# Performance work log

Hardware: AMD Instinct MI355X
Metric: run time of the kernel (lower is better)

Reference implementation:

```python
import jax, jax.numpy as jnp
import numpy as np

B, C, PC, P = 64, 32, 128, 2048
N = B * C * PC          # 262144 graph nodes
E = 2097152             # ~8 edges per node


def _gcn(x, src, dst, n, W, b):
    # PyG GCNConv: add self loops, sym-normalized mean aggregation of x@W
    xw = x @ W
    sl = jnp.arange(n, dtype=src.dtype)
    s = jnp.concatenate([src, sl]); d = jnp.concatenate([dst, sl])
    deg = jax.ops.segment_sum(jnp.ones(d.shape, xw.dtype), d, num_segments=n)
    dinv = jax.lax.rsqrt(deg)  # deg >= 1 thanks to self loops
    norm = dinv[s] * dinv[d]
    return jax.ops.segment_sum(xw[s] * norm[:, None], d, num_segments=n) + b


def _gat(x, src, dst, n, W, a_src, a_dst, b):
    # PyG GATConv (heads=1): self loops, edge softmax over incoming edges
    xw = x @ W
    sl = jnp.arange(n, dtype=src.dtype)
    s = jnp.concatenate([src, sl]); d = jnp.concatenate([dst, sl])
    e = jax.nn.leaky_relu((xw @ a_src)[s] + (xw @ a_dst)[d], 0.2)
    m = jax.ops.segment_max(jax.lax.stop_gradient(e), d, num_segments=n)
    ex = jnp.exp(e - m[d])
    denom = jax.ops.segment_sum(ex, d, num_segments=n)
    alpha = ex / denom[d]
    return jax.ops.segment_sum(xw[s] * alpha[:, None], d, num_segments=n) + b


def _cross_edges(num_cross, batch_size):
    # faithful to get_c_adjacency: every ordered pair (i!=j) appears twice per graph
    ii, jj = np.meshgrid(np.arange(num_cross), np.arange(num_cross), indexing='ij')
    m = ii != jj
    s, d = ii[m], jj[m]
    s2 = np.concatenate([s, d]); d2 = np.concatenate([d, s])
    off = (np.arange(batch_size) * num_cross)[:, None]
    src = (s2[None] + off).reshape(-1)
    dst = (d2[None] + off).reshape(-1)
    return jnp.asarray(src, jnp.int32), jnp.asarray(dst, jnp.int32)


def _conv1d(x, W, b):
    y = jax.lax.conv_general_dilated(x, W, (2,), ((1, 1),), dimension_numbers=('NCH', 'OIH', 'NCH'))
    return y + b[None, :, None]


def _bn_eval(x, gamma, beta):
    # BatchNorm1d in eval mode with default running stats (mean 0, var 1)
    scale = gamma / np.float32(np.sqrt(1.0 + 1e-5))
    return x * scale[None, :, None] + beta[None, :, None]


def setup_inputs() -> dict:
    key = jax.random.key(0)
    ks = jax.random.split(key, 32)
    rn = lambda k, sh, s=0.1: (jax.random.normal(k, sh, jnp.float32) * s)
    return {
        'x': jax.random.normal(ks[0], (N, 19), jnp.float32),
        'edge_index': jax.random.randint(ks[1], (2, E), 0, N, jnp.int32),
        'points': jax.random.normal(ks[2], (B, 3, P), jnp.float32),
        'W1': rn(ks[3], (19, 32)), 'b1': rn(ks[4], (32,)),
        'W2': rn(ks[5], (32, 64)), 'b2': rn(ks[6], (64,)),
        'W3': rn(ks[7], (64, 64)), 'b3': rn(ks[8], (64,)),
        'Wg1': rn(ks[9], (64, 64)), 'asrc1': rn(ks[10], (64,)), 'adst1': rn(ks[11], (64,)), 'bg1': rn(ks[12], (64,)),
        'Wg2': rn(ks[13], (64, 64)), 'asrc2': rn(ks[14], (64,)), 'adst2': rn(ks[15], (64,)), 'bg2': rn(ks[16], (64,)),
        'c1W': rn(ks[17], (32, 3, 3)), 'c1b': rn(ks[18], (32,)),
        'g1': 1.0 + rn(ks[19], (32,)), 'be1': rn(ks[20], (32,)),
        'c2W': rn(ks[21], (64, 32, 3)), 'c2b': rn(ks[22], (64,)),
        'g2': 1.0 + rn(ks[23], (64,)), 'be2': rn(ks[24], (64,)),
        'c3W': rn(ks[25], (64, 64, 3)), 'c3b': rn(ks[26], (64,)),
        'Wl2': rn(ks[27], (64, 64)), 'bl2': rn(ks[28], (64,)),
        'Wl3': rn(ks[29], (64, 1)), 'bl3': rn(ks[30], (1,)),
        'batch_size': B, 'num_cross': C, 'num_pieces': PC,
    }


def reference(x, edge_index, points, W1, b1, W2, b2, W3, b3,
              Wg1, asrc1, adst1, bg1, Wg2, asrc2, adst2, bg2,
              c1W, c1b, g1, be1, c2W, c2b, g2, be2, c3W, c3b,
              Wl2, bl2, Wl3, bl3, batch_size, num_cross, num_pieces):
    src, dst = edge_index[0], edge_index[1]
    n = x.shape[0]
    h = jax.nn.relu(_gcn(x, src, dst, n, W1, b1))  # dropout is a no-op in eval
    h = jax.nn.leaky_relu(_gcn(h, src, dst, n, W2, b2), 0.01)
    h = jax.nn.leaky_relu(_gcn(h, src, dst, n, W3, b3), 0.01)
    h = _gat(h, src, dst, n, Wg1, asrc1, adst1, bg1)
    h = h.reshape(batch_size, num_cross, num_pieces, -1).mean(-2)  # [B, C, 64]
    s2, d2 = _cross_edges(num_cross, batch_size)
    h = _gat(h.reshape(batch_size * num_cross, 64), s2, d2, batch_size * num_cross, Wg2, asrc2, adst2, bg2)
    h = h.reshape(batch_size, num_cross, 64).mean(1)  # [B, 64]
    p = _bn_eval(jax.nn.leaky_relu(_conv1d(points, c1W, c1b), 0.01), g1, be1)
    p = _bn_eval(jax.nn.leaky_relu(_conv1d(p, c2W, c2b), 0.01), g2, be2)
    p = jax.nn.leaky_relu(_conv1d(p, c3W, c3b), 0.01).mean(-1)  # AdaptiveAvgPool1d(1).squeeze -> [B, 64]
    h = h + p
    h = jax.nn.leaky_relu(h @ Wl2 + bl2, 0.01)
    return jax.nn.sigmoid(h @ Wl3 + bl3)  # [B, 1]
```

## Files before the change

### kernel.cpp

```cpp
#include <hip/hip_runtime.h>
#include <cstdint>
#include <cstddef>

#define NN 262144
#define EE 2097152
#define BB 64
#define CCROSS 32
#define PCC 128
#define PP 2048
#define NBUCK 256
#define BCAP 12288

typedef _Float16 f16;
typedef __attribute__((ext_vector_type(2))) _Float16 f16x2;
typedef __attribute__((ext_vector_type(4))) _Float16 f16x4;
typedef __attribute__((ext_vector_type(8))) _Float16 f16x8;
typedef __attribute__((ext_vector_type(4))) float f32x4;

static __device__ __forceinline__ float lrelu(float x, float s) { return x > 0.f ? x : s * x; }

#if __has_builtin(__builtin_amdgcn_fdot2)
static __device__ __forceinline__ float dot2f(unsigned x, unsigned w, float c) {
    return __builtin_amdgcn_fdot2(__builtin_bit_cast(f16x2, x), __builtin_bit_cast(f16x2, w), c, false);
}
#else
static __device__ __forceinline__ float dot2f(unsigned x, unsigned w, float c) {
    f16x2 a = __builtin_bit_cast(f16x2, x);
    f16x2 b = __builtin_bit_cast(f16x2, w);
    return fmaf((float)a[0], (float)b[0], fmaf((float)a[1], (float)b[1], c));
}
#endif

__global__ __launch_bounds__(256) void bucket_a_k(const int* __restrict__ src, const int* __restrict__ dst,
                                                  unsigned* __restrict__ buckets, int* __restrict__ gcnt) {
    __shared__ int hist[NBUCK];
    __shared__ int base[NBUCK];
    __shared__ unsigned short rankbuf[8192];
    const int tid = threadIdx.x;
    const int e0 = blockIdx.x * 8192;
    hist[tid] = 0;
    __syncthreads();
    for (int i = tid; i < 8192; i += 256) {
        int d = dst[e0 + i];
        rankbuf[i] = (unsigned short)atomicAdd(&hist[d >> 10], 1);
    }
    __syncthreads();
    base[tid] = tid * BCAP + atomicAdd(&gcnt[tid], hist[tid]);
    __syncthreads();
    for (int i = tid; i < 8192; i += 256) {
        int s = src[e0 + i];
        int d = dst[e0 + i];
        int b = d >> 10;
        buckets[base[b] + rankbuf[i]] = ((unsigned)s << 10) | (unsigned)(d & 1023);
    }
}

__global__ void bucket_scan_k(const int* __restrict__ gcnt, int* __restrict__ bbase, int* __restrict__ rp) {
    __shared__ int tmp[256];
    int tid = threadIdx.x;
    int v = gcnt[tid];
    tmp[tid] = v;
    __syncthreads();
    for (int off = 1; off < 256; off <<= 1) {
        int t = (tid >= off) ? tmp[tid - off] : 0;
        __syncthreads();
        tmp[tid] += t;
        __syncthreads();
    }
    bbase[tid] = tmp[tid] - v;
    if (tid == 0) rp[NN] = EE;
}

__global__ __launch_bounds__(256) void bucket_b_k(const unsigned* __restrict__ buckets, const int* __restrict__ gcnt,
                                                  const int* __restrict__ bbase, int* __restrict__ rp,
                                                  float* __restrict__ dinv, int* __restrict__ col) {
    __shared__ int cnt[1024];
    __shared__ int scan[1024];
    __shared__ int wsum[256];
    const int b = blockIdx.x;
    const int tid = threadIdx.x;
    int n = gcnt[b];
    if (n > BCAP) n = BCAP;
    const unsigned* eb = buckets + (size_t)b * BCAP;
    const int gb = bbase[b];
    for (int i = tid; i < 1024; i += 256) cnt[i] = 0;
    __syncthreads();
    for (int i = tid; i < n; i += 256) atomicAdd(&cnt[eb[i] & 1023], 1);
    __syncthreads();
    int b4 = tid * 4;
    int c0 = cnt[b4], c1 = cnt[b4 + 1], c2 = cnt[b4 + 2], c3 = cnt[b4 + 3];
    int tsum = c0 + c1 + c2 + c3;
    wsum[tid] = tsum;
    __syncthreads();
    for (int off = 1; off < 256; off <<= 1) {
        int t = (tid >= off) ? wsum[tid - off] : 0;
        __syncthreads();
        wsum[tid] += t;
        __syncthreads();
    }
    int excl = wsum[tid] - tsum;
    scan[b4] = excl;
    scan[b4 + 1] = excl + c0;
    scan[b4 + 2] = excl + c0 + c1;
    scan[b4 + 3] = excl + c0 + c1 + c2;
    int vbase = b * 1024 + b4;
    rp[vbase + 0] = gb + scan[b4 + 0];
    rp[vbase + 1] = gb + scan[b4 + 1];
    rp[vbase + 2] = gb + scan[b4 + 2];
    rp[vbase + 3] = gb + scan[b4 + 3];
    dinv[vbase + 0] = rsqrtf((float)(c0 + 1));
    dinv[vbase + 1] = rsqrtf((float)(c1 + 1));
    dinv[vbase + 2] = rsqrtf((float)(c2 + 1));
    dinv[vbase + 3] = rsqrtf((float)(c3 + 1));
    __syncthreads();
    for (int i = tid; i < 1024; i += 256) cnt[i] = 0;
    __syncthreads();
    for (int i = tid; i < n; i += 256) {
        unsigned p = eb[i];
        int dl = p & 1023;
        int r = atomicAdd(&cnt[dl], 1);
        col[gb + scan[dl] + r] = (int)(p >> 10);
    }
}

__global__ void zprep_k(const float* __restrict__ x, const float* __restrict__ dinv, f16* __restrict__ z) {
    int v = blockIdx.x * 256 + threadIdx.x;
    if (v >= NN) return;
    float dv = dinv[v];
    const float* xr = x + (size_t)v * 19;
    float vv[20];
#pragma unroll
    for (int k = 0; k < 19; k++) vv[k] = dv * xr[k];
    vv[19] = 0.f;
    f16x4* zr = (f16x4*)(z + (size_t)v * 32);
#pragma unroll
    for (int c = 0; c < 5; c++) {
        f16x4 t = {(f16)vv[4 * c], (f16)vv[4 * c + 1], (f16)vv[4 * c + 2], (f16)vv[4 * c + 3]};
        zr[c] = t;
    }
    f16x4 zz = {(f16)0.f, (f16)0.f, (f16)0.f, (f16)0.f};
#pragma unroll
    for (int c = 5; c < 8; c++) zr[c] = zz;
}

#define ZSTR1 36
template <int KINR, int KOUT, int ACT>
__global__ __launch_bounds__(256) void fused_agg_gemm_k(const f16* __restrict__ z, const int* __restrict__ rp,
                                                        const int* __restrict__ col, const float* __restrict__ Wg,
                                                        const float* __restrict__ dinv, const float* __restrict__ bias,
                                                        f16* __restrict__ zout) {
    constexpr int NO = KOUT / 4;
    __shared__ float Wl[32 * KOUT];
    __shared__ float zrow[64 * ZSTR1];
    const int tid = threadIdx.x;
    for (int i = tid; i < 32 * KOUT; i += 256) Wl[i] = (i < KINR * KOUT) ? Wg[i] : 0.f;

    const int r = tid >> 2;
    const int idx = tid & 3;
    const int v = blockIdx.x * 64 + r;
    const f16x8* z8 = (const f16x8*)z;
    f16x8 a = z8[(size_t)v * 4 + idx];
    float acc8[8];
#pragma unroll
    for (int j = 0; j < 8; j++) acc8[j] = (float)a[j];
    int st = rp[v], e = rp[v + 1];
    int i = st;
    for (; i + 4 <= e; i += 4) {
        int u0 = col[i], u1 = col[i + 1], u2 = col[i + 2], u3 = col[i + 3];
        f16x8 a0 = z8[(size_t)u0 * 4 + idx];
        f16x8 a1 = z8[(size_t)u1 * 4 + idx];
        f16x8 a2 = z8[(size_t)u2 * 4 + idx];
        f16x8 a3 = z8[(size_t)u3 * 4 + idx];
#pragma unroll
        for (int j = 0; j < 8; j++)
            acc8[j] += ((float)a0[j] + (float)a1[j]) + ((float)a2[j] + (float)a3[j]);
    }
    for (; i < e; i++) {
        f16x8 aa = z8[(size_t)col[i] * 4 + idx];
#pragma unroll
        for (int j = 0; j < 8; j++) acc8[j] += (float)aa[j];
    }
    float4 s0, s1;
    s0.x = acc8[0]; s0.y = acc8[1]; s0.z = acc8[2]; s0.w = acc8[3];
    s1.x = acc8[4]; s1.y = acc8[5]; s1.z = acc8[6]; s1.w = acc8[7];
    *(float4*)&zrow[r * ZSTR1 + idx * 8] = s0;
    *(float4*)&zrow[r * ZSTR1 + idx * 8 + 4] = s1;
    __syncthreads();

    float acc[NO];
#pragma unroll
    for (int j = 0; j < NO; j++) acc[j] = 0.f;
#pragma unroll 4
    for (int k = 0; k < 32; k++) {
        float zv = zrow[r * ZSTR1 + k];
        const float* wr = Wl + k * KOUT + NO * idx;
#pragma unroll
        for (int j = 0; j < NO; j++) acc[j] = fmaf(zv, wr[j], acc[j]);
    }
    float dv = dinv[v];
    f16 hv[NO];
#pragma unroll
    for (int j = 0; j < NO; j++) {
        float o = dv * acc[j] + bias[NO * idx + j];
        o = (ACT == 0) ? fmaxf(o, 0.f) : lrelu(o, 0.01f);
        hv[j] = (f16)(o * dv);
    }
    if constexpr (NO == 8) {
        f16x8 h = {hv[0], hv[1], hv[2], hv[3], hv[4], hv[5], hv[6], hv[7]};
        *(f16x8*)(zout + (size_t)v * KOUT + NO * idx) = h;
    } else {
        f16x8 h0 = {hv[0], hv[1], hv[2], hv[3], hv[4], hv[5], hv[6], hv[7]};
        f16x8 h1 = {hv[8], hv[9], hv[10], hv[11], hv[12], hv[13], hv[14], hv[15]};
        f16x8* yo = (f16x8*)(zout + (size_t)v * KOUT + NO * idx);
        yo[0] = h0; yo[1] = h1;
    }
}

__global__ void pack_w_k(const float* __restrict__ W, f16* __restrict__ out) {
    int o = blockIdx.x * 256 + threadIdx.x;
    if (o >= 4096) return;
    int frag = o >> 9;
    int kt = frag >> 2;
    int c = frag & 3;
    int idx = o & 511;
    int l = idx >> 3;
    int j = idx & 7;
    int k = kt * 32 + ((l >> 4) << 3) + j;
    int n = 16 * c + (l & 15);
    out[o] = (f16)W[k * 64 + n];
}

__global__ void pack_c2_k(const float* __restrict__ W, f16* __restrict__ out) {
    int o = blockIdx.x * 256 + threadIdx.x;
    if (o >= 64 * 96) return;
    int ch = o / 96, r = o - ch * 96;
    int k = r >> 5, ci = r & 31;
    out[o] = (f16)W[ch * 96 + ci * 3 + k];
}

__global__ void pack_c3_k(const float* __restrict__ W, f16* __restrict__ out) {
    int o = blockIdx.x * 256 + threadIdx.x;
    if (o >= 64 * 192) return;
    int ch = o / 192, r = o - ch * 192;
    int k = r >> 6, ci = r & 63;
    out[o] = (f16)W[ch * 192 + ci * 3 + k];
}

#define HSTR 72
__global__ __launch_bounds__(256) void gemm3_gat_k(const f16* __restrict__ y, const int* __restrict__ rp,
                                                   const int* __restrict__ col, const f16* __restrict__ w3p,
                                                   const float* __restrict__ dinv, const float* __restrict__ b3,
                                                   const f16* __restrict__ wgp, const float* __restrict__ av,
                                                   const float* __restrict__ ad, f16* __restrict__ xw,
                                                   float* __restrict__ es, float* __restrict__ ed) {
    __shared__ f16 zin[64 * HSTR];
    __shared__ f16 hh[64 * HSTR];
    const int tid = threadIdx.x;
    const int v0 = blockIdx.x * 64;
    {
        const int row = tid >> 2;
        const int idx = tid & 3;
        const int v = v0 + row;
        const f16x8* y8 = (const f16x8*)y;
        f16x8 s0 = y8[(size_t)v * 8 + idx * 2];
        f16x8 s1 = y8[(size_t)v * 8 + idx * 2 + 1];
        float acc[16];
#pragma unroll
        for (int j = 0; j < 8; j++) { acc[j] = (float)s0[j]; acc[8 + j] = (float)s1[j]; }
        int s = rp[v], e = rp[v + 1];
        int i = s;
        for (; i + 2 <= e; i += 2) {
            int u0 = col[i], u1 = col[i + 1];
            f16x8 a0 = y8[(size_t)u0 * 8 + idx * 2];
            f16x8 a1 = y8[(size_t)u0 * 8 + idx * 2 + 1];
            f16x8 b0 = y8[(size_t)u1 * 8 + idx * 2];
            f16x8 b1 = y8[(size_t)u1 * 8 + idx * 2 + 1];
#pragma unroll
            for (int j = 0; j < 8; j++) {
                acc[j] += (float)a0[j] + (float)b0[j];
                acc[8 + j] += (float)a1[j] + (float)b1[j];
            }
        }
        for (; i < e; i++) {
            int u = col[i];
            f16x8 a0 = y8[(size_t)u * 8 + idx * 2];
            f16x8 a1 = y8[(size_t)u * 8 + idx * 2 + 1];
#pragma unroll
            for (int j = 0; j < 8; j++) { acc[j] += (float)a0[j]; acc[8 + j] += (float)a1[j]; }
        }
        f16x8 o0, o1;
#pragma unroll
        for (int j = 0; j < 8; j++) { o0[j] = (f16)acc[j]; o1[j] = (f16)acc[8 + j]; }
        *(f16x8*)&zin[row * HSTR + idx * 16] = o0;
        *(f16x8*)&zin[row * HSTR + idx * 16 + 8] = o1;
    }
    __syncthreads();

    const int w = tid >> 6;
    const int l = tid & 63;
    const int m = l & 15;
    const int q = l >> 4;
    const int r0 = 16 * w;

    f32x4 acc0 = {0.f, 0.f, 0.f, 0.f}, acc1 = acc0, acc2 = acc0, acc3 = acc0;
#pragma unroll
    for (int kt = 0; kt < 2; kt++) {
        f16x8 afrag = *(const f16x8*)&zin[(r0 + m) * HSTR + kt * 32 + q * 8];
        f16x8 b0 = *(const f16x8*)&w3p[((kt * 4 + 0) << 9) + l * 8];
        f16x8 b1 = *(const f16x8*)&w3p[((kt * 4 + 1) << 9) + l * 8];
        f16x8 b2 = *(const f16x8*)&w3p[((kt * 4 + 2) << 9) + l * 8];
        f16x8 b3f = *(const f16x8*)&w3p[((kt * 4 + 3) << 9) + l * 8];
        acc0 = __builtin_amdgcn_mfma_f32_16x16x32_f16(afrag, b0, acc0, 0, 0, 0);
        acc1 = __builtin_amdgcn_mfma_f32_16x16x32_f16(afrag, b1, acc1, 0, 0, 0);
        acc2 = __builtin_amdgcn_mfma_f32_16x16x32_f16(afrag, b2, acc2, 0, 0, 0);
        acc3 = __builtin_amdgcn_mfma_f32_16x16x32_f16(afrag, b3f, acc3, 0, 0, 0);
    }
    {
        float dv0 = dinv[v0 + r0 + q * 4 + 0];
        float dv1 = dinv[v0 + r0 + q * 4 + 1];
        float dv2 = dinv[v0 + r0 + q * 4 + 2];
        float dv3 = dinv[v0 + r0 + q * 4 + 3];
#pragma unroll
        for (int c = 0; c < 4; c++) {
            const f32x4* ac = (c == 0) ? &acc0 : (c == 1) ? &acc1 : (c == 2) ? &acc2 : &acc3;
            float bb = b3[16 * c + m];
            hh[(r0 + q * 4 + 0) * HSTR + 16 * c + m] = (f16)lrelu(dv0 * (*ac)[0] + bb, 0.01f);
            hh[(r0 + q * 4 + 1) * HSTR + 16 * c + m] = (f16)lrelu(dv1 * (*ac)[1] + bb, 0.01f);
            hh[(r0 + q * 4 + 2) * HSTR + 16 * c + m] = (f16)lrelu(dv2 * (*ac)[2] + bb, 0.01f);
            hh[(r0 + q * 4 + 3) * HSTR + 16 * c + m] = (f16)lrelu(dv3 * (*ac)[3] + bb, 0.01f);
        }
    }
    __syncthreads();

    acc0 = (f32x4){0.f, 0.f, 0.f, 0.f}; acc1 = acc0; acc2 = acc0; acc3 = acc0;
#pragma unroll
    for (int kt = 0; kt < 2; kt++) {
        f16x8 afrag = *(const f16x8*)&hh[(r0 + m) * HSTR + kt * 32 + q * 8];
        f16x8 b0 = *(const f16x8*)&wgp[((kt * 4 + 0) << 9) + l * 8];
        f16x8 b1 = *(const f16x8*)&wgp[((kt * 4 + 1) << 9) + l * 8];
        f16x8 b2 = *(const f16x8*)&wgp[((kt * 4 + 2) << 9) + l * 8];
        f16x8 b3f = *(const f16x8*)&wgp[((kt * 4 + 3) << 9) + l * 8];
        acc0 = __builtin_amdgcn_mfma_f32_16x16x32_f16(afrag, b0, acc0, 0, 0, 0);
        acc1 = __builtin_amdgcn_mfma_f32_16x16x32_f16(afrag, b1, acc1, 0, 0, 0);
        acc2 = __builtin_amdgcn_mfma_f32_16x16x32_f16(afrag, b2, acc2, 0, 0, 0);
        acc3 = __builtin_amdgcn_mfma_f32_16x16x32_f16(afrag, b3f, acc3, 0, 0, 0);
    }
    {
        float e1[4] = {0.f, 0.f, 0.f, 0.f}, e2[4] = {0.f, 0.f, 0.f, 0.f};
#pragma unroll
        for (int c = 0; c < 4; c++) {
            const f32x4* ac = (c == 0) ? &acc0 : (c == 1) ? &acc1 : (c == 2) ? &acc2 : &acc3;
            float a1 = av[16 * c + m];
            float d1 = ad[16 * c + m];
#pragma unroll
            for (int reg = 0; reg < 4; reg++) {
                float g = (*ac)[reg];
                e1[reg] = fmaf(g, a1, e1[reg]);
                e2[reg] = fmaf(g, d1, e2[reg]);
                xw[(size_t)(v0 + r0 + q * 4 + reg) * 64 + 16 * c + m] = (f16)g;
            }
        }
#pragma unroll
        for (int reg = 0; reg < 4; reg++) {
            e1[reg] += __shfl_xor(e1[reg], 1); e1[reg] += __shfl_xor(e1[reg], 2);
            e1[reg] += __shfl_xor(e1[reg], 4); e1[reg] += __shfl_xor(e1[reg], 8);
            e2[reg] += __shfl_xor(e2[reg], 1); e2[reg] += __shfl_xor(e2[reg], 2);
            e2[reg] += __shfl_xor(e2[reg], 4); e2[reg] += __shfl_xor(e2[reg], 8);
        }
        if (m == 0) {
#pragma unroll
            for (int reg = 0; reg < 4; reg++) {
                es[v0 + r0 + q * 4 + reg] = e1[reg];
                ed[v0 + r0 + q * 4 + reg] = e2[reg];
            }
        }
    }
}

__global__ void gat_w_k(const float* __restrict__ es, const float* __restrict__ ed,
                        const int* __restrict__ rp, const int* __restrict__ col,
                        f16* __restrict__ ewi, float* __restrict__ wsi) {
    int v = blockIdx.x * 256 + threadIdx.x;
    if (v >= NN) return;
    float edv = ed[v];
    float eself = lrelu(es[v] + edv, 0.2f);
    float m = eself;
    int s = rp[v], e = rp[v + 1];
    int i = s;
    float lg[32];
    for (; i + 4 <= e; i += 4) {
        int u0 = col[i], u1 = col[i + 1], u2 = col[i + 2], u3 = col[i + 3];
        float t0 = lrelu(es[u0] + edv, 0.2f);
        float t1 = lrelu(es[u1] + edv, 0.2f);
        float t2 = lrelu(es[u2] + edv, 0.2f);
        float t3 = lrelu(es[u3] + edv, 0.2f);
        int k = i - s;
        if (k + 3 < 32) { lg[k] = t0; lg[k + 1] = t1; lg[k + 2] = t2; lg[k + 3] = t3; }
        m = fmaxf(m, fmaxf(fmaxf(t0, t1), fmaxf(t2, t3)));
    }
    for (; i < e; i++) {
        float t = lrelu(es[col[i]] + edv, 0.2f);
        int k = i - s;
        if (k < 32) lg[k] = t;
        m = fmaxf(m, t);
    }
    float wsl = __expf(eself - m);
    float den = wsl;
    for (i = s; i < e; i++) {
        int k = i - s;
        float t = (k < 32) ? lg[k] : lrelu(es[col[i]] + edv, 0.2f);
        float w = __expf(t - m);
        if (k < 32) lg[k] = w;
        den += w;
    }
    float inv = 1.f / den;
    for (i = s; i < e; i++) {
        int k = i - s;
        float w = (k < 32) ? lg[k] : __expf(lrelu(es[col[i]] + edv, 0.2f) - m);
        ewi[i] = (f16)(w * inv);
    }
    wsi[v] = wsl * inv;
}

__global__ __launch_bounds__(256) void gat_agg_pool_k(const f16* __restrict__ y, const int* __restrict__ rp,
                                                      const int* __restrict__ col, const f16* __restrict__ ewi,
                                                      const float* __restrict__ wsi,
                                                      const float* __restrict__ bias, float* __restrict__ pooled) {
    __shared__ float sred[32 * 68];
    const int g = blockIdx.x;
    const int tid = threadIdx.x;
    const int idx = tid & 7;
    const int slot = tid >> 3;
    const f16x8* y8 = (const f16x8*)y;
    float acc[8];
#pragma unroll
    for (int j = 0; j < 8; j++) acc[j] = 0.f;

#pragma unroll
    for (int pass = 0; pass < 4; pass++) {
        const int v = g * 128 + pass * 32 + slot;
        float ws = wsi[v];
        f16x8 self = y8[(size_t)v * 8 + idx];
#pragma unroll
        for (int j = 0; j < 8; j++) acc[j] = fmaf(ws, (float)self[j], acc[j]);
    }

    const int s = rp[g * 128];
    const int e = rp[g * 128 + 128];
    int i = s + slot;
    for (; i + 96 < e; i += 128) {
        int u0 = col[i], u1 = col[i + 32], u2 = col[i + 64], u3 = col[i + 96];
        float w0 = (float)ewi[i], w1 = (float)ewi[i + 32], w2 = (float)ewi[i + 64], w3 = (float)ewi[i + 96];
        f16x8 a0 = y8[(size_t)u0 * 8 + idx];
        f16x8 a1 = y8[(size_t)u1 * 8 + idx];
        f16x8 a2 = y8[(size_t)u2 * 8 + idx];
        f16x8 a3 = y8[(size_t)u3 * 8 + idx];
#pragma unroll
        for (int j = 0; j < 8; j++)
            acc[j] = fmaf(w0, (float)a0[j], fmaf(w1, (float)a1[j], fmaf(w2, (float)a2[j], fmaf(w3, (float)a3[j], acc[j]))));
    }
    for (; i < e; i += 32) {
        int u = col[i];
        float w = (float)ewi[i];
        f16x8 a = y8[(size_t)u * 8 + idx];
#pragma unroll
        for (int j = 0; j < 8; j++) acc[j] = fmaf(w, (float)a[j], acc[j]);
    }

#pragma unroll
    for (int j = 0; j < 8; j++) sred[slot * 68 + idx * 8 + j] = acc[j];
    __syncthreads();
    if (tid < 64) {
        float s2 = 0.f;
#pragma unroll
        for (int k = 0; k < 32; k++) s2 += sred[k * 68 + tid];
        pooled[(size_t)g * 64 + tid] = s2 * (1.f / 128.f) + bias[tid];
    }
}

__global__ void pool_cross_k(const float* __restrict__ in, float* __restrict__ out) {
    int gid = blockIdx.x * 64 + threadIdx.x;
    if (gid >= BB * 64) return;
    int f = gid & 63, b = gid >> 6;
    const float* p = in + (size_t)b * CCROSS * 64 + f;
    float s = 0.f;
#pragma unroll
    for (int i = 0; i < CCROSS; i++) s += p[(size_t)i * 64];
    out[gid] = s * (1.f / 32.f);
}

template <int KIN, int KOUT>
__global__ void gat_gemm_k(const float* __restrict__ x, const float* __restrict__ W,
                           float* __restrict__ y, const float* __restrict__ av, const float* __restrict__ ad,
                           float* __restrict__ es, float* __restrict__ ed, int n) {
    int v = blockIdx.x * 256 + threadIdx.x;
    if (v >= n) return;
    const float* xr = x + (size_t)v * KIN;
    float acc[KOUT];
#pragma unroll
    for (int j = 0; j < KOUT; j++) acc[j] = 0.f;
#pragma unroll 2
    for (int k = 0; k < KIN; k++) {
        float xv = xr[k];
#pragma unroll
        for (int j = 0; j < KOUT; j++) acc[j] = fmaf(xv, W[k * KOUT + j], acc[j]);
    }
    float e1 = 0.f, e2 = 0.f;
    float4* y4 = (float4*)(y + (size_t)v * KOUT);
#pragma unroll
    for (int j4 = 0; j4 < KOUT / 4; j4++) {
        float4 t;
        t.x = acc[4 * j4 + 0]; t.y = acc[4 * j4 + 1]; t.z = acc[4 * j4 + 2]; t.w = acc[4 * j4 + 3];
        y4[j4] = t;
        e1 = fmaf(t.x, av[4 * j4 + 0], e1); e1 = fmaf(t.y, av[4 * j4 + 1], e1);
        e1 = fmaf(t.z, av[4 * j4 + 2], e1); e1 = fmaf(t.w, av[4 * j4 + 3], e1);
        e2 = fmaf(t.x, ad[4 * j4 + 0], e2); e2 = fmaf(t.y, ad[4 * j4 + 1], e2);
        e2 = fmaf(t.z, ad[4 * j4 + 2], e2); e2 = fmaf(t.w, ad[4 * j4 + 3], e2);
    }
    es[v] = e1; ed[v] = e2;
}

__global__ void cross_att_k(const float* __restrict__ xw, const float* __restrict__ es,
                            const float* __restrict__ ed, const float* __restrict__ bg,
                            float* __restrict__ out) {
    int gid = blockIdx.x * 256 + threadIdx.x;
    if (gid >= BB * CCROSS * 64) return;
    int f = gid & 63;
    int d = (gid >> 6) & 31;
    int g = gid >> 11;
    int base = g * CCROSS;
    float edd = ed[base + d];
    float m = -1e30f;
#pragma unroll
    for (int s = 0; s < CCROSS; s++) {
        float e = lrelu(es[base + s] + edd, 0.2f);
        m = fmaxf(m, e);
    }
    float den = 0.f, acc = 0.f;
#pragma unroll
    for (int s = 0; s < CCROSS; s++) {
        float e = lrelu(es[base + s] + edd, 0.2f);
        float w = __expf(e - m) * ((s == d) ? 1.f : 2.f);
        den += w;
        acc = fmaf(w, xw[(size_t)(base + s) * 64 + f], acc);
    }
    out[gid] = acc / den + bg[f];
}

__global__ __launch_bounds__(256) void conv_fused_k(
        const float* __restrict__ pts, const float* __restrict__ c1W, const float* __restrict__ c1b,
        const float* __restrict__ g1, const float* __restrict__ be1,
        const f16* __restrict__ w2p, const float* __restrict__ c2b,
        const float* __restrict__ g2, const float* __restrict__ be2,
        const f16* __restrict__ w3pc, const float* __restrict__ c3b,
        float* __restrict__ partials) {
    __shared__ __align__(16) float s0[3 * 264];
    __shared__ __align__(16) f16 s1T[132 * 32];
    __shared__ __align__(16) f16 s2T[66 * 64];
    __shared__ float sred[256];

    const int b = blockIdx.x >> 3;
    const int q = blockIdx.x & 7;
    const int tid = threadIdx.x;
    const float bnscale = 0.99999500003749968f;

    const int lo0 = 256 * q - 7;
    for (int t = tid; t < 3 * 263; t += 256) {
        int c = t / 263, j = t - c * 263;
        int p = lo0 + j;
        s0[c * 264 + j] = (p >= 0 && p < PP) ? pts[((size_t)b * 3 + c) * PP + p] : 0.f;
    }
    __syncthreads();

    {
        const int ch = tid & 31;
        const int j0 = tid >> 5;
        float wv[9];
        const float* wg = c1W + ch * 9;
#pragma unroll
        for (int t = 0; t < 9; t++) wv[t] = wg[t];
        const float bs = c1b[ch];
        const float gs = g1[ch] * bnscale;
        const float bt = be1[ch];
        const int lo1 = 128 * q - 3;
        for (int j = j0; j < 131; j += 8) {
            int p1 = lo1 + j;
            float v = 0.f;
            if (p1 >= 0 && p1 < 1024) {
                const float* x0 = s0 + 2 * j;
                float a0 = bs, a1 = 0.f, a2 = 0.f;
#pragma unroll
                for (int c = 0; c < 3; c++) {
                    float2 x01 = *(const float2*)(x0 + c * 264);
                    float x2v = x0[c * 264 + 2];
                    a0 = fmaf(x01.x, wv[c * 3 + 0], a0);
                    a1 = fmaf(x01.y, wv[c * 3 + 1], a1);
                    a2 = fmaf(x2v, wv[c * 3 + 2], a2);
                }
                float acc = a0 + a1 + a2;
                acc = lrelu(acc, 0.01f);
                v = fmaf(acc, gs, bt);
            }
            s1T[j * 32 + ch] = (f16)v;
        }
    }
    __syncthreads();

    {
        const int ch = tid & 63;
        const int jg = tid >> 6;
        unsigned wr[48];
        const uint4* wp = (const uint4*)(w2p + (size_t)ch * 96);
#pragma unroll
        for (int t = 0; t < 12; t++) {
            uint4 u = wp[t];
            wr[4 * t + 0] = u.x; wr[4 * t + 1] = u.y; wr[4 * t + 2] = u.z; wr[4 * t + 3] = u.w;
        }
        const float bs = c2b[ch];
        const float gs = g2[ch] * bnscale;
        const float bt = be2[ch];
        const int lo2v = 64 * q - 1;
        for (int j = jg; j < 65; j += 4) {
            float ak[3] = {bs, 0.f, 0.f};
#pragma unroll
            for (int k = 0; k < 3; k++) {
                const uint4* xp = (const uint4*)(s1T + (2 * j + k) * 32);
                uint4 x0 = xp[0], x1 = xp[1], x2 = xp[2], x3 = xp[3];
                float a = ak[k];
                a = dot2f(x0.x, wr[k * 16 + 0], a);
                a = dot2f(x0.y, wr[k * 16 + 1], a);
                a = dot2f(x0.z, wr[k * 16 + 2], a);
                a = dot2f(x0.w, wr[k * 16 + 3], a);
                a = dot2f(x1.x, wr[k * 16 + 4], a);
                a = dot2f(x1.y, wr[k * 16 + 5], a);
                a = dot2f(x1.z, wr[k * 16 + 6], a);
                a = dot2f(x1.w, wr[k * 16 + 7], a);
                a = dot2f(x2.x, wr[k * 16 + 8], a);
                a = dot2f(x2.y, wr[k * 16 + 9], a);
                a = dot2f(x2.z, wr[k * 16 + 10], a);
                a = dot2f(x2.w, wr[k * 16 + 11], a);
                a = dot2f(x3.x, wr[k * 16 + 12], a);
                a = dot2f(x3.y, wr[k * 16 + 13], a);
                a = dot2f(x3.z, wr[k * 16 + 14], a);
                a = dot2f(x3.w, wr[k * 16 + 15], a);
                ak[k] = a;
            }
            float acc = ak[0] + ak[1] + ak[2];
            int p2 = lo2v + j;
            float v = 0.f;
            if (p2 >= 0 && p2 < 512) v = fmaf(lrelu(acc, 0.01f), gs, bt);
            s2T[j * 64 + ch] = (f16)v;
        }
    }
    __syncthreads();

    {
        const int ch = tid & 63;
        const int jg = tid >> 6;
        unsigned wr[96];
        const uint4* wp = (const uint4*)(w3pc + (size_t)ch * 192);
#pragma unroll
        for (int t = 0; t < 24; t++) {
            uint4 u = wp[t];
            wr[4 * t + 0] = u.x; wr[4 * t + 1] = u.y; wr[4 * t + 2] = u.z; wr[4 * t + 3] = u.w;
        }
        const float bs = c3b[ch];
        float psum = 0.f;
        for (int j = jg; j < 32; j += 4) {
            float ak[3] = {bs, 0.f, 0.f};
#pragma unroll
            for (int k = 0; k < 3; k++) {
                const uint4* xp = (const uint4*)(s2T + (2 * j + k) * 64);
                float a = ak[k];
#pragma unroll
                for (int t = 0; t < 8; t++) {
                    uint4 xv = xp[t];
                    a = dot2f(xv.x, wr[k * 32 + 4 * t + 0], a);
                    a = dot2f(xv.y, wr[k * 32 + 4 * t + 1], a);
                    a = dot2f(xv.z, wr[k * 32 + 4 * t + 2], a);
                    a = dot2f(xv.w, wr[k * 32 + 4 * t + 3], a);
                }
                ak[k] = a;
            }
            psum += lrelu(ak[0] + ak[1] + ak[2], 0.01f);
        }
        sred[tid] = psum;
    }
    __syncthreads();
    if (tid < 64) {
        float s = sred[tid] + sred[tid + 64] + sred[tid + 128] + sred[tid + 192];
        partials[((size_t)b * 8 + q) * 64 + tid] = s;
    }
}

__global__ void head_k(const float* __restrict__ hG, const float* __restrict__ partials,
                       const float* __restrict__ Wl2, const float* __restrict__ bl2,
                       const float* __restrict__ Wl3, const float* __restrict__ bl3,
                       float* __restrict__ out) {
    int b = blockIdx.x;
    int f = threadIdx.x;
    __shared__ float sh[64];
    float p = 0.f;
#pragma unroll
    for (int q = 0; q < 8; q++) p += partials[((size_t)b * 8 + q) * 64 + f];
    float h = hG[b * 64 + f] + p * (1.f / 256.f);
    sh[f] = h;
    __syncthreads();
    float acc = bl2[f];
#pragma unroll
    for (int k = 0; k < 64; k++) acc = fmaf(sh[k], Wl2[k * 64 + f], acc);
    acc = lrelu(acc, 0.01f);
    float pr = acc * Wl3[f];
#pragma unroll
    for (int off = 32; off > 0; off >>= 1) pr += __shfl_down(pr, off, 64);
    if (f == 0) out[b] = 1.f / (1.f + __expf(-(pr + bl3[0])));
}

extern "C" void kernel_launch(void* const* d_in, const int* in_sizes, int n_in,
                              void* d_out, int out_size, void* d_ws, size_t ws_size,
                              hipStream_t stream) {
    const float* x = (const float*)d_in[0];
    const int* ei = (const int*)d_in[1];
    const float* points = (const float*)d_in[2];
    const float* W1 = (const float*)d_in[3];
    const float* b1 = (const float*)d_in[4];
    const float* W2 = (const float*)d_in[5];
    const float* b2 = (const float*)d_in[6];
    const float* W3 = (const float*)d_in[7];
    const float* b3 = (const float*)d_in[8];
    const float* Wg1 = (const float*)d_in[9];
    const float* asrc1 = (const float*)d_in[10];
    const float* adst1 = (const float*)d_in[11];
    const float* bg1 = (const float*)d_in[12];
    const float* Wg2 = (const float*)d_in[13];
    const float* asrc2 = (const float*)d_in[14];
    const float* adst2 = (const float*)d_in[15];
    const float* bg2 = (const float*)d_in[16];
    const float* c1W = (const float*)d_in[17];
    const float* c1b = (const float*)d_in[18];
    const float* g1 = (const float*)d_in[19];
    const float* be1 = (const float*)d_in[20];
    const float* c2W = (const float*)d_in[21];
    const float* c2b = (const float*)d_in[22];
    const float* g2 = (const float*)d_in[23];
    const float* be2 = (const float*)d_in[24];
    const float* c3W = (const float*)d_in[25];
    const float* c3b = (const float*)d_in[26];
    const float* Wl2 = (const float*)d_in[27];
    const float* bl2 = (const float*)d_in[28];
    const float* Wl3 = (const float*)d_in[29];
    const float* bl3 = (const float*)d_in[30];

    const int* src = ei;
    const int* dst = ei + EE;

    char* w = (char*)d_ws;
    size_t off = 0;
    auto A = [&](size_t bytes) -> void* {
        void* p = w + off;
        off = (off + bytes + 255) & ~(size_t)255;
        return p;
    };
    int* colb = (int*)A((size_t)EE * 4);
    int* rp = (int*)A((size_t)(NN + 1) * 4);
    int* gcnt = (int*)A(NBUCK * 4);
    int* bbase = (int*)A(NBUCK * 4);
    float* dinv = (float*)A((size_t)NN * 4);
    float* bufA = (float*)A((size_t)NN * 64 * 4);
    f16* bufH1 = (f16*)A((size_t)NN * 64 * 2);
    f16* bufH2 = (f16*)A((size_t)NN * 64 * 2);
    f16* ewi = (f16*)A((size_t)EE * 2);
    float* wsi = (float*)A((size_t)NN * 4);
    float* es = (float*)A((size_t)NN * 4);
    float* edv = (float*)A((size_t)NN * 4);
    f16* w3p = (f16*)A(4096 * 2);
    f16* wgp = (f16*)A(4096 * 2);
    f16* wc2p = (f16*)A(64 * 96 * 2);
    f16* wc3p = (f16*)A(64 * 192 * 2);
    float* pooled = (float*)A((size_t)BB * CCROSS * 64 * 4);
    float* xw2 = (float*)A((size_t)BB * CCROSS * 64 * 4);
    float* es2 = (float*)A((size_t)BB * CCROSS * 4);
    float* ed2 = (float*)A((size_t)BB * CCROSS * 4);
    float* crosso = (float*)A((size_t)BB * CCROSS * 64 * 4);
    float* hG = (float*)A((size_t)BB * 64 * 4);
    float* partials = (float*)A((size_t)BB * 8 * 64 * 4);

    unsigned* buckets = (unsigned*)bufA;

    hipMemsetAsync(gcnt, 0, NBUCK * 4, stream);
    bucket_a_k<<<EE / 8192, 256, 0, stream>>>(src, dst, buckets, gcnt);
    bucket_scan_k<<<1, 256, 0, stream>>>(gcnt, bbase, rp);
    bucket_b_k<<<NBUCK, 256, 0, stream>>>(buckets, gcnt, bbase, rp, dinv, colb);

    pack_c2_k<<<24, 256, 0, stream>>>(c2W, wc2p);
    pack_c3_k<<<48, 256, 0, stream>>>(c3W, wc3p);
    conv_fused_k<<<BB * 8, 256, 0, stream>>>(points, c1W, c1b, g1, be1, wc2p, c2b, g2, be2, wc3p, c3b, partials);
    pack_w_k<<<16, 256, 0, stream>>>(W3, w3p);
    pack_w_k<<<16, 256, 0, stream>>>(Wg1, wgp);

    zprep_k<<<NN / 256, 256, 0, stream>>>(x, dinv, bufH1);
    fused_agg_gemm_k<19, 32, 0><<<NN / 64, 256, 0, stream>>>(bufH1, rp, colb, W1, dinv, b1, bufH2);
    fused_agg_gemm_k<32, 64, 1><<<NN / 64, 256, 0, stream>>>(bufH2, rp, colb, W2, dinv, b2, bufH1);
    gemm3_gat_k<<<NN / 64, 256, 0, stream>>>(bufH1, rp, colb, w3p, dinv, b3, wgp, asrc1, adst1,
                                             bufH2, es, edv);

    gat_w_k<<<NN / 256, 256, 0, stream>>>(es, edv, rp, colb, ewi, wsi);
    gat_agg_pool_k<<<BB * CCROSS, 256, 0, stream>>>(bufH2, rp, colb, ewi, wsi, bg1, pooled);

    gat_gemm_k<64, 64><<<(BB * CCROSS) / 256, 256, 0, stream>>>(pooled, Wg2, xw2, asrc2, adst2, es2, ed2, BB * CCROSS);
    cross_att_k<<<(BB * CCROSS * 64) / 256, 256, 0, stream>>>(xw2, es2, ed2, bg2, crosso);
    pool_cross_k<<<BB, 64, 0, stream>>>(crosso, hG);

    head_k<<<BB, 64, 0, stream>>>(hG, partials, Wl2, bl2, Wl3, bl3, (float*)d_out);
}
```

Before: 473.8 us.

## Balance edge aggregation across threads with edge-chunked split and LDS float atomics

The neighbor gather in the fused GCN3+GAT kernel now splits the block's CSR edge range evenly across 32 slots of 8 threads each, instead of giving each node to 4 threads. Each slot finds its starting row by binary search over a shared copy of the row pointers, sums per-row partials, and adds them into an fp32 LDS buffer with atomics. The goal is to remove load imbalance from uneven node degrees and to issue more independent gathers per thread. In exchange it adds LDS atomics, an extra fp32 staging pass, another barrier and more shared memory, though hh now reuses the fp32 buffer.

After: 572.2 us. 1.21x slower.

```diff
diff --git a/kernel.cpp b/kernel.cpp
--- a/kernel.cpp
+++ b/kernel.cpp
@@ -247,52 +247,78 @@
 }
 
 #define HSTR 72
+#define Z32S 68
 __global__ __launch_bounds__(256) void gemm3_gat_k(const f16* __restrict__ y, const int* __restrict__ rp,
                                                    const int* __restrict__ col, const f16* __restrict__ w3p,
                                                    const float* __restrict__ dinv, const float* __restrict__ b3,
                                                    const f16* __restrict__ wgp, const float* __restrict__ av,
                                                    const float* __restrict__ ad, f16* __restrict__ xw,
                                                    float* __restrict__ es, float* __restrict__ ed) {
+    __shared__ float zin32[64 * Z32S];
     __shared__ f16 zin[64 * HSTR];
-    __shared__ f16 hh[64 * HSTR];
+    __shared__ int rpl[65];
+    f16* hh = (f16*)zin32;
+
     const int tid = threadIdx.x;
     const int v0 = blockIdx.x * 64;
+    const f16x8* y8 = (const f16x8*)y;
+
+    if (tid < 65) rpl[tid] = rp[v0 + tid];
     {
-        const int row = tid >> 2;
-        const int idx = tid & 3;
-        const int v = v0 + row;
-        const f16x8* y8 = (const f16x8*)y;
-        f16x8 s0 = y8[(size_t)v * 8 + idx * 2];
-        f16x8 s1 = y8[(size_t)v * 8 + idx * 2 + 1];
-        float acc[16];
-#pragma unroll
-        for (int j = 0; j < 8; j++) { acc[j] = (float)s0[j]; acc[8 + j] = (float)s1[j]; }
-        int s = rp[v], e = rp[v + 1];
-        int i = s;
-        for (; i + 2 <= e; i += 2) {
-            int u0 = col[i], u1 = col[i + 1];
-            f16x8 a0 = y8[(size_t)u0 * 8 + idx * 2];
-            f16x8 a1 = y8[(size_t)u0 * 8 + idx * 2 + 1];
-            f16x8 b0 = y8[(size_t)u1 * 8 + idx * 2];
-            f16x8 b1 = y8[(size_t)u1 * 8 + idx * 2 + 1];
-#pragma unroll
-            for (int j = 0; j < 8; j++) {
-                acc[j] += (float)a0[j] + (float)b0[j];
-                acc[8 + j] += (float)a1[j] + (float)b1[j];
+        const int row = tid >> 2, qq = tid & 3;
+        const f16x8* yp = y8 + (size_t)(v0 + row) * 8 + qq * 2;
+        f16x8 s0 = yp[0], s1 = yp[1];
+        float* zr = &zin32[row * Z32S + qq * 16];
+#pragma unroll
+        for (int j = 0; j < 8; j++) { zr[j] = (float)s0[j]; zr[8 + j] = (float)s1[j]; }
+    }
+    __syncthreads();
+
+    {
+        const int slot = tid >> 3;
+        const int f = tid & 7;
+        const int sE = rpl[0], eE = rpl[64];
+        const int chunk = (eE - sE + 31) >> 5;
+        int i = sE + slot * chunk;
+        const int iend = min(i + chunk, eE);
+        if (i < iend) {
+            int lo = 0, hi = 64;
+            while (hi - lo > 1) { int mid = (lo + hi) >> 1; if (i >= rpl[mid]) lo = mid; else hi = mid; }
+            int r = lo;
+            while (i < iend) {
+                while (i >= rpl[r + 1]) r++;
+                const int rend = min(rpl[r + 1], iend);
+                float acc[8];
+#pragma unroll
+                for (int j = 0; j < 8; j++) acc[j] = 0.f;
+                for (; i + 2 <= rend; i += 2) {
+                    int u0 = col[i], u1 = col[i + 1];
+                    f16x8 a0 = y8[(size_t)u0 * 8 + f];
+                    f16x8 a1 = y8[(size_t)u1 * 8 + f];
+#pragma unroll
+                    for (int j = 0; j < 8; j++) acc[j] += (float)a0[j] + (float)a1[j];
+                }
+                for (; i < rend; i++) {
+                    f16x8 a = y8[(size_t)col[i] * 8 + f];
+#pragma unroll
+                    for (int j = 0; j < 8; j++) acc[j] += (float)a[j];
+                }
+                float* zr = &zin32[r * Z32S + f * 8];
+#pragma unroll
+                for (int j = 0; j < 8; j++) atomicAdd(&zr[j], acc[j]);
             }
         }
-        for (; i < e; i++) {
-            int u = col[i];
-            f16x8 a0 = y8[(size_t)u * 8 + idx * 2];
-            f16x8 a1 = y8[(size_t)u * 8 + idx * 2 + 1];
-#pragma unroll
-            for (int j = 0; j < 8; j++) { acc[j] += (float)a0[j]; acc[8 + j] += (float)a1[j]; }
-        }
+    }
+    __syncthreads();
+
+    {
+        const int row = tid >> 2, qq = tid & 3;
+        const float* zr = &zin32[row * Z32S + qq * 16];
         f16x8 o0, o1;
 #pragma unroll
-        for (int j = 0; j < 8; j++) { o0[j] = (f16)acc[j]; o1[j] = (f16)acc[8 + j]; }
-        *(f16x8*)&zin[row * HSTR + idx * 16] = o0;
-        *(f16x8*)&zin[row * HSTR + idx * 16 + 8] = o1;
+        for (int j = 0; j < 8; j++) { o0[j] = (f16)zr[j]; o1[j] = (f16)zr[8 + j]; }
+        *(f16x8*)&zin[row * HSTR + qq * 16] = o0;
+        *(f16x8*)&zin[row * HSTR + qq * 16 + 8] = o1;
     }
     __syncthreads();
 
```
